# Kernel tuning notes

Measured on AMD Instinct MI355X. Metric: run time of the kernel, lower is better.

## Reference

```python
import jax, jax.numpy as jnp
import numpy as np
from jax.scipy.special import logsumexp

EPROB = 0.01
PSEUDO = 1.0


def setup_inputs() -> dict:
    key = jax.random.key(0)
    ks = jax.random.split(key, 6)
    B, m, n, d = 16, 2000, 1000, 5000
    gexp = jax.random.normal(ks[0], (B, d), jnp.float32)
    # one-hot observed dosages for 2B haplotypes (batch is duplicated in forward)
    idx = jax.random.randint(ks[1], (2 * B, m), 0, 2)
    x_onehots = jax.nn.one_hot(idx, 2, dtype=jnp.float32)
    W = jax.random.normal(ks[2], (d, m), jnp.float32) * 0.02  # predictor Linear weight
    b = jax.random.normal(ks[3], (m,), jnp.float32) * 0.01    # predictor Linear bias
    ref_tensor = jax.random.randint(ks[4], (m, n), 0, 2).astype(jnp.int32)  # 0/1 ref dosages
    recomb_rates = jax.random.uniform(ks[5], (m,), jnp.float32, 1e-4, 0.1)
    return dict(gexp=gexp, x_onehots=x_onehots, W=W, b=b,
                ref_tensor=ref_tensor, recomb_rates=recomb_rates)


def reference(gexp, x_onehots, W, b, ref_tensor, recomb_rates):
    m, n = ref_tensor.shape
    logn = jnp.log(jnp.float32(n))
    lse = logsumexp

    # predictor -> per-site Bernoulli priors, duplicated across haplotype pairs
    one_p = jax.nn.sigmoid(gexp @ W + b)                  # [B, m]
    prior = jnp.stack([1.0 - one_p, one_p], axis=-1)      # [B, m, 2]
    log_phi = jnp.log(jnp.repeat(prior, 2, axis=0))       # [2B, m, 2] (interleaved dup)
    B2 = log_phi.shape[0]

    # emission table: log of [[1-e, e],[e, 1-e]] + pseudocount/n
    E = np.array([[1.0 - EPROB, EPROB], [EPROB, 1.0 - EPROB]], dtype=np.float64) + PSEUDO / n
    logE = jnp.asarray(np.log(E), jnp.float32)            # [2, 2]
    SE = logE[ref_tensor]                                 # [m, n, 2] state emissions

    x_t = jnp.transpose(x_onehots, (1, 0, 2))             # [m, B2, 2]
    phi_t = jnp.transpose(log_phi, (1, 0, 2))             # [m, B2, 2]
    # forward step i uses recomb_rates[i+1]; last step's update is discarded
    r_next = jnp.concatenate([recomb_rates[1:], jnp.full((1,), 0.5, jnp.float32)])

    # ---- forward HMM pass: builds fprobx_haplo [m, B2, n] ----
    def fwd_step(f, xs):
        SE_i, x_i, r = xs                                  # [n,2], [B2,2], []
        nxt = f + jnp.einsum('kl,bl->bk', SE_i, x_i)       # [B2, n]
        nxt = nxt - lse(nxt, axis=1, keepdims=True)
        tot = lse(nxt, axis=1) - logn                      # [B2]
        nr = jnp.log((1.0 - r) * jnp.exp(nxt) + r * jnp.exp(tot)[:, None])
        nr = nr - lse(nr, axis=1, keepdims=True)
        return nr, f

    f0 = jnp.zeros((B2, n), jnp.float32)
    _, fprobx = jax.lax.scan(fwd_step, f0, (SE, x_t, r_next))  # [m, B2, n]

    # ---- backward pass (reverse recursion), accumulating log p(x|e) ----
    def bwd_step(carry, xs):
        state, p_xe = carry                                # state == prevprob == nextprob
        f_i, SE_i, phi_i, x_i, r = xs
        dp = lse(f_i[:, :, None] + state[:, :, None] + SE_i[None], axis=1)  # [B2, 2]
        dpp = dp + phi_i
        dpn = dpp - lse(dpp, axis=1, keepdims=True)
        p_xe = p_xe + jnp.sum(dpn * x_i, axis=1)
        nn = lse(SE_i[None] + phi_i[:, None, :], axis=2)   # [B2, n]
        state = state + nn - lse(nn, axis=1, keepdims=True)
        tot = lse(state, axis=1) - logn
        nr = jnp.log((1.0 - r) * jnp.exp(state) + r * jnp.exp(tot)[:, None])
        nr = nr - lse(nr, axis=1, keepdims=True)
        return (nr, p_xe), None

    init = (jnp.zeros((B2, n), jnp.float32), jnp.zeros((B2,), jnp.float32))
    (_, p_xe), _ = jax.lax.scan(bwd_step, init,
                                (fprobx, SE, phi_t, x_t, recomb_rates), reverse=True)

    return -jnp.sum(p_xe)  # loss_fn (training=True path)
```

## Files before the change

kernel.cpp:

```cpp
#include <hip/hip_runtime.h>
#include <stdint.h>
#include <stddef.h>

static constexpr int MM   = 2000;
static constexpr int NN   = 1000;
static constexpr int NB2  = 32;
static constexpr int DDIM = 5000;
static constexpr int NPR  = 1008;
static constexpr int NG   = 500;
static constexpr int JB   = 8;
static constexpr int NBAT = MM/JB;
static constexpr int NCR  = 36;
static constexpr float EAV = 0.991f;
static constexpr float EBV = 0.011f;

typedef uint32_t u32x4 __attribute__((ext_vector_type(4)));
typedef uint32_t u32x2 __attribute__((ext_vector_type(2)));
typedef float    f32x2 __attribute__((ext_vector_type(2)));

__device__ __forceinline__ float rcp_fast(float x){ return __builtin_amdgcn_rcpf(x); }

__device__ __forceinline__ void barrier_lds_only(){
  __builtin_amdgcn_sched_barrier(0);
  asm volatile("s_waitcnt lgkmcnt(0)" ::: "memory");
  __builtin_amdgcn_s_barrier();
  __builtin_amdgcn_sched_barrier(0);
}

__device__ __forceinline__ void wave_total2(float &a, float &b){
  int xa, xb;
  xa = __builtin_amdgcn_update_dpp(0, __float_as_int(a), 0x111, 0xf, 0xf, true);
  xb = __builtin_amdgcn_update_dpp(0, __float_as_int(b), 0x111, 0xf, 0xf, true);
  a += __int_as_float(xa); b += __int_as_float(xb);
  xa = __builtin_amdgcn_update_dpp(0, __float_as_int(a), 0x112, 0xf, 0xf, true);
  xb = __builtin_amdgcn_update_dpp(0, __float_as_int(b), 0x112, 0xf, 0xf, true);
  a += __int_as_float(xa); b += __int_as_float(xb);
  xa = __builtin_amdgcn_update_dpp(0, __float_as_int(a), 0x114, 0xf, 0xf, true);
  xb = __builtin_amdgcn_update_dpp(0, __float_as_int(b), 0x114, 0xf, 0xf, true);
  a += __int_as_float(xa); b += __int_as_float(xb);
  xa = __builtin_amdgcn_update_dpp(0, __float_as_int(a), 0x118, 0xf, 0xf, true);
  xb = __builtin_amdgcn_update_dpp(0, __float_as_int(b), 0x118, 0xf, 0xf, true);
  a += __int_as_float(xa); b += __int_as_float(xb);
  xa = __builtin_amdgcn_update_dpp(0, __float_as_int(a), 0x142, 0xa, 0xf, false);
  xb = __builtin_amdgcn_update_dpp(0, __float_as_int(b), 0x142, 0xa, 0xf, false);
  a += __int_as_float(xa); b += __int_as_float(xb);
  xa = __builtin_amdgcn_update_dpp(0, __float_as_int(a), 0x143, 0xc, 0xf, false);
  xb = __builtin_amdgcn_update_dpp(0, __float_as_int(b), 0x143, 0xc, 0xf, false);
  a += __int_as_float(xa); b += __int_as_float(xb);
  a = __int_as_float(__builtin_amdgcn_readlane(__float_as_int(a), 63));
  b = __int_as_float(__builtin_amdgcn_readlane(__float_as_int(b), 63));
}

template<int C,int RM,int BM,bool BC>
__device__ __forceinline__ void dpp_stage8(float m[8]){
  int x[8];
  #pragma unroll
  for (int j = 0; j < 8; ++j)
    x[j] = __builtin_amdgcn_update_dpp(0, __float_as_int(m[j]), C, RM, BM, BC);
  #pragma unroll
  for (int j = 0; j < 8; ++j) m[j] += __int_as_float(x[j]);
}
__device__ __forceinline__ void wave_total8_63(float m[8]){
  dpp_stage8<0x111,0xf,0xf,true>(m);
  dpp_stage8<0x112,0xf,0xf,true>(m);
  dpp_stage8<0x114,0xf,0xf,true>(m);
  dpp_stage8<0x118,0xf,0xf,true>(m);
  dpp_stage8<0x142,0xa,0xf,false>(m);
  dpp_stage8<0x143,0xc,0xf,false>(m);
}

#define CCEL(A,i) ( ((i)&3)==0 ? (A)[(i)>>2].x : ((i)&3)==1 ? (A)[(i)>>2].y : \
                    ((i)&3)==2 ? (A)[(i)>>2].z : (A)[(i)>>2].w )

__global__ __launch_bounds__(64) void k_pack(const int* __restrict__ ref,
                                             uint64_t* __restrict__ pack,
                                             uint4* __restrict__ refB4){
  int g = blockIdx.x;
  int t = threadIdx.x;
  uint64_t wv = 0;
  for (int c = 0; c < 4; ++c){
    int i = g*4 + c;
    uint32_t m16 = 0;
    uint32_t d[4] = {0,0,0,0};
    #pragma unroll
    for (int j = 0; j < 16; ++j){
      int k = t*16 + j;
      uint32_t v = (k < NN) ? (uint32_t)(ref[(size_t)i*NN + k] & 1) : 0u;
      m16 |= v << j;
      d[j>>2] |= v << (8*(j&3));
    }
    wv |= (uint64_t)m16 << (16*c);
    refB4[(size_t)i*64 + t] = make_uint4(d[0],d[1],d[2],d[3]);
  }
  pack[(size_t)g*64 + t] = wv;
}

__global__ __launch_bounds__(64) void k_obs(const float* __restrict__ xoh,
                                            uint32_t* __restrict__ obsw){
  int b2 = blockIdx.x;
  int w  = threadIdx.x;
  uint32_t word = 0;
  int base = w*32;
  #pragma unroll 4
  for (int z = 0; z < 32; ++z){
    int i = base + z;
    if (i < MM){
      float x1 = xoh[(size_t)b2*MM*2 + (size_t)i*2 + 1];
      if (x1 > 0.5f) word |= 1u << z;
    }
  }
  obsw[b2*64 + w] = word;
}

__global__ __launch_bounds__(256) void k_prep2(const float* __restrict__ xoh,
                                               const float* __restrict__ recomb,
                                               float4* __restrict__ FC4){
  int idx = blockIdx.x*256 + threadIdx.x;
  if (idx < NB2*MM){
    int b2 = idx / MM, i = idx - b2*MM;
    float x1 = xoh[(size_t)b2*MM*2 + (size_t)i*2 + 1];
    bool obs = x1 > 0.5f;
    float c0 = obs ? EBV : EAV;
    float c1 = obs ? (EAV-EBV) : (EBV-EAV);
    float rn = (i+1 < MM) ? recomb[i+1] : 0.5f;
    FC4[(size_t)b2*MM + i] = make_float4(c0, c1, 1.0f - rn, rn/(float)NN);
  }
}

__global__ __launch_bounds__(256) void k_gemm(const float* __restrict__ gexp,
                                              const float* __restrict__ W,
                                              float* __restrict__ part){
  int cb = blockIdx.x;
  int c  = blockIdx.y;
  int t  = threadIdx.x;
  int d0 = (c*DDIM) >> 4, d1 = ((c+1)*DDIM) >> 4;
  int len = d1 - d0;
  __shared__ __align__(16) float lg[313*20];
  for (int bb = 0; bb < 16; ++bb)
    for (int dd = t; dd < len; dd += 256)
      lg[dd*20 + bb] = gexp[(size_t)bb*DDIM + d0 + dd];
  __syncthreads();
  int i = cb*256 + t;
  if (i < MM){
    float acc[16];
    #pragma unroll
    for (int bb = 0; bb < 16; ++bb) acc[bb] = 0.f;
    for (int dd = 0; dd < len; ++dd){
      float w = W[(size_t)(d0 + dd)*MM + i];
      const float4* lp = (const float4*)&lg[dd*20];
      float4 g0 = lp[0], g1 = lp[1], g2 = lp[2], g3 = lp[3];
      acc[0]  += g0.x*w; acc[1]  += g0.y*w; acc[2]  += g0.z*w; acc[3]  += g0.w*w;
      acc[4]  += g1.x*w; acc[5]  += g1.y*w; acc[6]  += g1.z*w; acc[7]  += g1.w*w;
      acc[8]  += g2.x*w; acc[9]  += g2.y*w; acc[10] += g2.z*w; acc[11] += g2.w*w;
      acc[12] += g3.x*w; acc[13] += g3.y*w; acc[14] += g3.z*w; acc[15] += g3.w*w;
    }
    #pragma unroll
    for (int bb = 0; bb < 16; ++bb)
      part[((size_t)c*16 + bb)*MM + i] = acc[bb];
  }
}

__global__ __launch_bounds__(256) void k_gemmreduce(const float* __restrict__ part,
                                                    const float* __restrict__ bias,
                                                    const float* __restrict__ recomb,
                                                    float* __restrict__ acc,
                                                    float4* __restrict__ BC4){
  int idx = blockIdx.x*256 + threadIdx.x;
  if (idx < 16*MM){
    float s = 0.f;
    #pragma unroll
    for (int c = 0; c < 16; ++c) s += part[(size_t)c*16*MM + idx];
    acc[idx] = s;
    int bb = idx / MM, i = idx - bb*MM;
    float z = s + bias[i];
    float p = rcp_fast(1.0f + __expf(-z));
    float v0 = EAV + (EBV-EAV)*p;
    float v1 = EBV + (EAV-EBV)*p;
    float r = recomb[i];
    BC4[idx] = make_float4(v0, v1 - v0, 1.0f - r, r/(float)NN);
  }
}

__global__ __launch_bounds__(64) void k_ctab(const uint4* __restrict__ refB4,
                                             const float4* __restrict__ FC4,
                                             const float4* __restrict__ BC4,
                                             float* __restrict__ Cout){
  int wid  = blockIdx.x;
  int lane = threadIdx.x;
  int chain = wid / NBAT;
  int nb    = wid - chain*NBAT;
  int DIR = (chain < 32) ? 1 : -1;
  int b2  = chain & 31;
  const float4* ctab = (chain < 32) ? (FC4 + (size_t)b2*MM) : (BC4 + (size_t)(b2>>1)*MM);
  int start = (DIR > 0) ? 0 : (MM-1);

  f32x2 e[8][8];
  #pragma unroll
  for (int m = 0; m < 8; ++m){
    int site = start + DIR*(nb*JB + m);
    uint4 by = refB4[(size_t)site*64 + lane];
    float4 cc = ctab[site];
    f32x2 c0p; c0p.x = cc.x; c0p.y = cc.x;
    f32x2 c1p; c1p.x = cc.y; c1p.y = cc.y;
    uint32_t rw[4] = {by.x, by.y, by.z, by.w};
    #pragma unroll
    for (int q = 0; q < 4; ++q){
      f32x2 b01, b23;
      b01.x = (float)( rw[q]        & 0xFFu);
      b01.y = (float)((rw[q] >> 8)  & 0xFFu);
      b23.x = (float)((rw[q] >> 16) & 0xFFu);
      b23.y = (float)( rw[q] >> 24);
      e[m][2*q]   = c0p + c1p*b01;
      e[m][2*q+1] = c0p + c1p*b23;
    }
  }
  const float mlo = (lane < 63) ? 1.0f : 0.0f;
  const float mhi = (lane < 62) ? 1.0f : 0.0f;

  __shared__ float red[64*NCR];
  int cnt = 0;
  #pragma unroll
  for (int l = 0; l < 8; ++l){
    f32x2 c[8];
    #pragma unroll
    for (int q = 0; q < 8; ++q){
      f32x2 mk; mk.x = (q < 4) ? mlo : mhi; mk.y = mk.x;
      c[q] = e[l][q] * mk;
    }
    #pragma unroll
    for (int jj = l; jj < 8; ++jj){
      if (jj > l){
        #pragma unroll
        for (int q = 0; q < 8; ++q) c[q] = c[q] * e[jj][q];
      }
      f32x2 s0 = (c[0]+c[1]) + (c[2]+c[3]);
      f32x2 s1 = (c[4]+c[5]) + (c[6]+c[7]);
      f32x2 ss = s0 + s1;
      red[lane*NCR + cnt] = ss.x + ss.y;
      ++cnt;
    }
  }
  __syncthreads();
  if (lane < NCR){
    float s = 0.f;
    #pragma unroll
    for (int k = 0; k < 64; ++k) s += red[k*NCR + lane];
    Cout[(size_t)wid*NCR + lane] = s;
  }
}

template<int DIR>
__device__ void run_chain4(const uint32_t* __restrict__ refW,
                           const float4* __restrict__ ctab,
                           const float* __restrict__ Crec,
                           uint16_t* __restrict__ outp,
                           int b2, int w, int lane,
                           float4* lds_ctab, float* lds_C, float* partb){
  for (int idx = w*64 + lane; idx < MM; idx += 256)
    lds_ctab[idx] = ctab[idx];
  for (int idx = w*64 + lane; idx < NBAT*NCR; idx += 256)
    lds_C[idx] = Crec[idx];
  __syncthreads();

  const float mv  = ((w < 3) || (lane < 58)) ? 1.0f : 0.0f;
  const bool doSt = (w < 3) || (lane < 60);

  const ptrdiff_t rstep = (ptrdiff_t)DIR * 256;
  const uint32_t* rp = refW + ((DIR > 0) ? 0 : (ptrdiff_t)(MM-1)*256) + w*64 + lane;
  const ptrdiff_t ostep = (ptrdiff_t)DIR * NB2 * NPR;
  uint16_t* op = outp + (size_t)b2*NPR
               + ((DIR > 0) ? (size_t)0 : (size_t)(MM-1)*(size_t)NB2*NPR)
               + (size_t)w*256 + (size_t)lane*4;

  uint32_t A[8], Bv[8];
  #pragma unroll
  for (int k = 0; k < 8; ++k) A[k]  = rp[(ptrdiff_t)k*rstep];
  #pragma unroll
  for (int k = 0; k < 8; ++k) Bv[k] = rp[(ptrdiff_t)(k+8)*rstep];

  int ci = (DIR > 0) ? 0 : (MM-1);

  float4 cur8[8];
  #pragma unroll
  for (int k = 0; k < 8; ++k) cur8[k] = lds_ctab[ci + DIR*k];

  f32x2 g0, g1;
  g0.x = 0.f; g0.y = 0.f; g1.x = 0.f; g1.y = 0.f;
  float dd      = 1.0f/(float)NN;
  float az_prev = 0.0f;
  int buf = 0;
  constexpr int CO[8] = {0,8,15,21,26,30,33,35};

  #pragma unroll 2
  for (int n = 0; n < NBAT; ++n){
    uint32_t Cv[8];
    #pragma unroll
    for (int k = 0; k < 8; ++k) Cv[k] = rp[(ptrdiff_t)(8*n + 16 + k)*rstep];
    float4 nx8[8];
    {
      int cin = (n < NBAT-1) ? (ci + DIR*8) : ci;
      #pragma unroll
      for (int k = 0; k < 8; ++k) nx8[k] = lds_ctab[cin + DIR*k];
    }
    float4 CC[9];
    {
      const float4* crp = (const float4*)(lds_C + n*NCR);
      #pragma unroll
      for (int r = 0; r < 9; ++r) CC[r] = crp[r];
    }
    f32x2 e0[8], e1[8];
    #pragma unroll
    for (int k = 0; k < 8; ++k){
      uint32_t rw = A[k];
      f32x2 c0p; c0p.x = cur8[k].x; c0p.y = cur8[k].x;
      f32x2 c1p; c1p.x = cur8[k].y; c1p.y = cur8[k].y;
      f32x2 b01, b23;
      b01.x = (float)( rw        & 0xFFu);
      b01.y = (float)((rw >> 8)  & 0xFFu);
      b23.x = (float)((rw >> 16) & 0xFFu);
      b23.y = (float)( rw >> 24);
      e0[k] = c0p + c1p*b01;
      e1[k] = c0p + c1p*b23;
    }
    float m[8];
    {
      f32x2 c0 = g0*e0[0], c1 = g1*e1[0];
      f32x2 hv = c0 + c1;
      m[0] = hv.x + hv.y;
      #pragma unroll
      for (int k = 1; k < 8; ++k){
        c0 = c0*e0[k]; c1 = c1*e1[k];
        f32x2 h = c0 + c1;
        m[k] = h.x + h.y;
      }
    }
    wave_total8_63(m);
    if (lane == 63){
      #pragma unroll
      for (int j = 0; j < 8; ++j) partb[buf*32 + j*4 + w] = m[j];
    }
    barrier_lds_only();
    float M[8];
    #pragma unroll
    for (int j = 0; j < 8; ++j){
      const float4 pp = *(const float4*)(partb + buf*32 + j*4);
      M[j] = (pp.x + pp.y) + (pp.z + pp.w);
    }
    float cf[8];
    float azp = az_prev;
    float R = 1.0f;
    #pragma unroll
    for (int j = 0; j < 8; ++j){
      if (j > 0){
        float azm = cur8[j-1].z;
        azp *= azm;
        #pragma unroll
        for (int l = 0; l < 8; ++l) if (l < j) cf[l] *= azm;
      }
      cf[j] = dd;
      float az_j = (j == 0) ? az_prev : cur8[j-1].z;
      float dm = dd * mv;
      f32x2 azv; azv.x = az_j; azv.y = az_j;
      f32x2 dmv; dmv.x = dm;   dmv.y = dm;
      f32x2 t0 = g0*azv + dmv;
      f32x2 t1 = g1*azv + dmv;
      if (doSt){
        u32x2 v;
        v.x = __builtin_amdgcn_perm(__float_as_uint(t0.y), __float_as_uint(t0.x), 0x07060302u);
        v.y = __builtin_amdgcn_perm(__float_as_uint(t1.y), __float_as_uint(t1.x), 0x07060302u);
        *(u32x2*)op = v;
      }
      op += ostep;
      g0 = t0*e0[j];
      g1 = t1*e1[j];
      float T = azp * M[j];
      #pragma unroll
      for (int l = 0; l < 8; ++l) if (l <= j) T = fmaf(cf[l], CCEL(CC, CO[l] + (j-l)), T);
      R = T;
      dd = cur8[j].w * R;
    }
    float s = rcp_fast(R);
    f32x2 sp; sp.x = s; sp.y = s;
    g0 = g0*sp; g1 = g1*sp;
    dd *= s;
    az_prev = cur8[7].z;
    ci += DIR*8;
    buf ^= 1;
    #pragma unroll
    for (int k = 0; k < 8; ++k){ A[k] = Bv[k]; Bv[k] = Cv[k]; }
    #pragma unroll
    for (int k = 0; k < 8; ++k) cur8[k] = nx8[k];
  }
}

__global__ __launch_bounds__(256, 1) void k_chains(const uint4* __restrict__ refB4,
                                                   const float4* __restrict__ FC4,
                                                   const float4* __restrict__ BC4,
                                                   const float* __restrict__ Cw,
                                                   uint16_t* __restrict__ F,
                                                   uint16_t* __restrict__ S){
  __shared__ __align__(16) float4 lds_ctab[MM];
  __shared__ __align__(16) float lds_C[NBAT*NCR];
  __shared__ __align__(16) float partb[64];
  int lane = threadIdx.x & 63;
  int w    = threadIdx.x >> 6;
  int blk  = blockIdx.x;
  int b2   = blk & 31;
  const uint32_t* refW = (const uint32_t*)refB4;
  const float* Crec = Cw + (size_t)blk*NBAT*NCR;
  if (blk < 32) run_chain4<1>(refW, FC4 + (size_t)b2*MM, Crec, F, b2, w, lane,
                              lds_ctab, lds_C, partb);
  else          run_chain4<-1>(refW, BC4 + (size_t)(b2>>1)*MM, Crec, S, b2, w, lane,
                               lds_ctab, lds_C, partb);
}

__global__ __launch_bounds__(256) void k_sites(const uint16_t* __restrict__ F,
                                               const uint16_t* __restrict__ S,
                                               const uint64_t* __restrict__ pack,
                                               const uint32_t* __restrict__ obsw,
                                               const float* __restrict__ acc,
                                               const float* __restrict__ bias,
                                               float* __restrict__ terms){
  int lane = threadIdx.x & 63;
  int wid  = threadIdx.x >> 6;
  int s    = blockIdx.x*4 + wid;
  int i    = s >> 5;
  int b2   = s & 31;
  uint4 f0 = make_uint4(0,0,0,0), f1 = f0, s0 = f0, s1 = f0;
  if (lane < 63){
    size_t off = ((size_t)i*NB2 + b2)*NPR + lane*16;
    const uint4* fp = (const uint4*)(F + off);
    const uint4* sp = (const uint4*)(S + off);
    f0 = fp[0]; f1 = fp[1];
    s0 = sp[0]; s1 = sp[1];
  }
  uint32_t m16 = (uint32_t)(pack[(size_t)(i>>2)*64 + lane] >> (16*(i&3))) & 0xFFFFu;

  uint32_t fa[8] = {f0.x,f0.y,f0.z,f0.w,f1.x,f1.y,f1.z,f1.w};
  uint32_t sa[8] = {s0.x,s0.y,s0.z,s0.w,s1.x,s1.y,s1.z,s1.w};
  float Tt = 0.f, Tb = 0.f;
  #pragma unroll
  for (int q = 0; q < 8; ++q){
    float flo = __uint_as_float(fa[q] << 16);
    float fhi = __uint_as_float(fa[q] & 0xFFFF0000u);
    float slo = __uint_as_float(sa[q] << 16);
    float shi = __uint_as_float(sa[q] & 0xFFFF0000u);
    float pl = flo*slo, ph = fhi*shi;
    Tt += pl + ph;
    Tb += (((m16 >> (2*q)) & 1u) ? pl : 0.f) + (((m16 >> (2*q+1)) & 1u) ? ph : 0.f);
  }
  wave_total2(Tt, Tb);
  if (lane == 0){
    uint32_t obsb = (obsw[b2*64 + (i>>5)] >> (i & 31)) & 1u;
    float z = acc[(size_t)(b2 >> 1)*MM + i] + bias[i];
    float p = rcp_fast(1.0f + __expf(-z));
    float A = Tt - Tb, B = Tb;
    float d0 = EAV*A + EBV*B;
    float d1 = EBV*A + EAV*B;
    float w0 = d0*(1.0f - p), w1 = d1*p;
    float term = __logf((obsb ? w1 : w0) * rcp_fast(w0 + w1));
    terms[s] = term;
  }
}

__global__ __launch_bounds__(256) void k_final(const float* __restrict__ terms,
                                               float* __restrict__ out){
  __shared__ float red[256];
  float s = 0.f;
  for (int idx = threadIdx.x; idx < MM*NB2; idx += 256) s += terms[idx];
  red[threadIdx.x] = s;
  __syncthreads();
  for (int st = 128; st > 0; st >>= 1){
    if (threadIdx.x < st) red[threadIdx.x] += red[threadIdx.x + st];
    __syncthreads();
  }
  if (threadIdx.x == 0) out[0] = -red[0];
}

extern "C" void kernel_launch(void* const* d_in, const int* in_sizes, int n_in,
                              void* d_out, int out_size, void* d_ws, size_t ws_size,
                              hipStream_t stream){
  const float* gexp   = (const float*)d_in[0];
  const float* xoh    = (const float*)d_in[1];
  const float* W      = (const float*)d_in[2];
  const float* bias   = (const float*)d_in[3];
  const int*   ref    = (const int*)d_in[4];
  const float* recomb = (const float*)d_in[5];
  float* out = (float*)d_out;
  char* ws = (char*)d_ws;

  const size_t stateBytes = (size_t)MM*NB2*NPR*2;
  size_t offF    = 0;
  size_t offS    = offF + stateBytes;
  size_t offPack = offS + stateBytes;
  size_t offObs  = offPack + (size_t)NG*64*8;
  size_t offPart = offObs + 32*64*4;
  size_t offTerm = offPart + (size_t)16*16*MM*4;
  size_t offAcc  = offTerm + (size_t)MM*NB2*4;
  size_t offRefB = offAcc + (size_t)16*MM*4;
  size_t offFC4  = offRefB + (size_t)(MM+32)*1024;
  size_t offBC4  = offFC4 + (size_t)NB2*MM*16;

  uint16_t* Fb   = (uint16_t*)(ws + offF);
  uint16_t* Sb   = (uint16_t*)(ws + offS);
  uint64_t* pack = (uint64_t*)(ws + offPack);
  uint32_t* obsw = (uint32_t*)(ws + offObs);
  float*    part = (float*)(ws + offPart);
  float*    Cw   = (float*)(ws + offPart);
  float*    term = (float*)(ws + offTerm);
  float*    accp = (float*)(ws + offAcc);
  uint4*    refB = (uint4*)(ws + offRefB) + 16*64;
  float4*   FC4  = (float4*)(ws + offFC4);
  float4*   BC4  = (float4*)(ws + offBC4);

  hipLaunchKernelGGL(k_pack, dim3(NG), dim3(64), 0, stream, ref, pack, refB);
  hipLaunchKernelGGL(k_obs, dim3(32), dim3(64), 0, stream, xoh, obsw);
  hipLaunchKernelGGL(k_prep2, dim3((NB2*MM+255)/256), dim3(256), 0, stream, xoh, recomb, FC4);
  hipLaunchKernelGGL(k_gemm, dim3(8,16), dim3(256), 0, stream, gexp, W, part);
  hipLaunchKernelGGL(k_gemmreduce, dim3(125), dim3(256), 0, stream, part, bias, recomb, accp, BC4);
  hipLaunchKernelGGL(k_ctab, dim3(64*NBAT), dim3(64), 0, stream, refB, FC4, BC4, Cw);
  hipLaunchKernelGGL(k_chains, dim3(64), dim3(256), 0, stream, refB, FC4, BC4, Cw, Fb, Sb);
  hipLaunchKernelGGL(k_sites, dim3(MM*NB2/4), dim3(256), 0, stream, Fb, Sb, pack, obsw, accp, bias, term);
  hipLaunchKernelGGL(k_final, dim3(1), dim3(256), 0, stream, term, out);
}
```

Measured before the change: 600.1 us.

## Split each HMM chain across eight waves with two states per lane

```diff
diff --git a/kernel.cpp b/kernel.cpp
--- a/kernel.cpp
+++ b/kernel.cpp
@@ -250,27 +250,27 @@
 }
 
 template<int DIR>
-__device__ void run_chain4(const uint32_t* __restrict__ refW,
+__device__ void run_chain8(const uint16_t* __restrict__ refH,
                            const float4* __restrict__ ctab,
                            const float* __restrict__ Crec,
                            uint16_t* __restrict__ outp,
                            int b2, int w, int lane,
                            float4* lds_ctab, float* lds_C, float* partb){
-  for (int idx = w*64 + lane; idx < MM; idx += 256)
-    lds_ctab[idx] = ctab[idx];
-  for (int idx = w*64 + lane; idx < NBAT*NCR; idx += 256)
-    lds_C[idx] = Crec[idx];
+  int tid = w*64 + lane;
+  for (int idx = tid; idx < MM; idx += 512) lds_ctab[idx] = ctab[idx];
+  for (int idx = tid; idx < NBAT*NCR; idx += 512) lds_C[idx] = Crec[idx];
   __syncthreads();
 
-  const float mv  = ((w < 3) || (lane < 58)) ? 1.0f : 0.0f;
-  const bool doSt = (w < 3) || (lane < 60);
-
-  const ptrdiff_t rstep = (ptrdiff_t)DIR * 256;
-  const uint32_t* rp = refW + ((DIR > 0) ? 0 : (ptrdiff_t)(MM-1)*256) + w*64 + lane;
+  const int st0 = w*128 + lane*2;
+  const float mv  = (st0 < NN)  ? 1.0f : 0.0f;
+  const bool doSt = (st0 < NPR);
+
+  const ptrdiff_t rstep = (ptrdiff_t)DIR * 512;
+  const uint16_t* rp = refH + ((DIR > 0) ? 0 : (ptrdiff_t)(MM-1)*512) + tid;
   const ptrdiff_t ostep = (ptrdiff_t)DIR * NB2 * NPR;
   uint16_t* op = outp + (size_t)b2*NPR
                + ((DIR > 0) ? (size_t)0 : (size_t)(MM-1)*(size_t)NB2*NPR)
-               + (size_t)w*256 + (size_t)lane*4;
+               + (size_t)st0;
 
   uint32_t A[8], Bv[8];
   #pragma unroll
@@ -284,8 +284,7 @@
   #pragma unroll
   for (int k = 0; k < 8; ++k) cur8[k] = lds_ctab[ci + DIR*k];
 
-  f32x2 g0, g1;
-  g0.x = 0.f; g0.y = 0.f; g1.x = 0.f; g1.y = 0.f;
+  f32x2 g; g.x = 0.f; g.y = 0.f;
   float dd      = 1.0f/(float)NN;
   float az_prev = 0.0f;
   int buf = 0;
@@ -308,44 +307,44 @@
       #pragma unroll
       for (int r = 0; r < 9; ++r) CC[r] = crp[r];
     }
-    f32x2 e0[8], e1[8];
+    f32x2 e[8];
     #pragma unroll
     for (int k = 0; k < 8; ++k){
       uint32_t rw = A[k];
+      f32x2 b01;
+      b01.x = (float)( rw        & 0xFFu);
+      b01.y = (float)( rw >> 8);
       f32x2 c0p; c0p.x = cur8[k].x; c0p.y = cur8[k].x;
       f32x2 c1p; c1p.x = cur8[k].y; c1p.y = cur8[k].y;
-      f32x2 b01, b23;
-      b01.x = (float)( rw        & 0xFFu);
-      b01.y = (float)((rw >> 8)  & 0xFFu);
-      b23.x = (float)((rw >> 16) & 0xFFu);
-      b23.y = (float)( rw >> 24);
-      e0[k] = c0p + c1p*b01;
-      e1[k] = c0p + c1p*b23;
+      e[k] = c0p + c1p*b01;
     }
     float m[8];
     {
-      f32x2 c0 = g0*e0[0], c1 = g1*e1[0];
-      f32x2 hv = c0 + c1;
-      m[0] = hv.x + hv.y;
+      f32x2 c = g*e[0];
+      m[0] = c.x + c.y;
       #pragma unroll
       for (int k = 1; k < 8; ++k){
-        c0 = c0*e0[k]; c1 = c1*e1[k];
-        f32x2 h = c0 + c1;
-        m[k] = h.x + h.y;
+        c = c*e[k];
+        m[k] = c.x + c.y;
       }
     }
     wave_total8_63(m);
     if (lane == 63){
       #pragma unroll
-      for (int j = 0; j < 8; ++j) partb[buf*32 + j*4 + w] = m[j];
+      for (int j = 0; j < 8; ++j) partb[buf*64 + j*8 + w] = m[j];
     }
     barrier_lds_only();
     float M[8];
-    #pragma unroll
-    for (int j = 0; j < 8; ++j){
-      const float4 pp = *(const float4*)(partb + buf*32 + j*4);
-      M[j] = (pp.x + pp.y) + (pp.z + pp.w);
-    }
+    {
+      int ll = lane & 7;
+      const float4* pb = (const float4*)(partb + buf*64 + ll*8);
+      float4 pa = pb[0], pc = pb[1];
+      float msum = ((pa.x+pa.y)+(pa.z+pa.w)) + ((pc.x+pc.y)+(pc.z+pc.w));
+      #pragma unroll
+      for (int j = 0; j < 8; ++j)
+        M[j] = __int_as_float(__builtin_amdgcn_readlane(__float_as_int(msum), j));
+    }
+    uint32_t vst[8];
     float cf[8];
     float azp = az_prev;
     float R = 1.0f;
@@ -362,26 +361,27 @@
       float dm = dd * mv;
       f32x2 azv; azv.x = az_j; azv.y = az_j;
       f32x2 dmv; dmv.x = dm;   dmv.y = dm;
-      f32x2 t0 = g0*azv + dmv;
-      f32x2 t1 = g1*azv + dmv;
-      if (doSt){
-        u32x2 v;
-        v.x = __builtin_amdgcn_perm(__float_as_uint(t0.y), __float_as_uint(t0.x), 0x07060302u);
-        v.y = __builtin_amdgcn_perm(__float_as_uint(t1.y), __float_as_uint(t1.x), 0x07060302u);
-        *(u32x2*)op = v;
-      }
-      op += ostep;
-      g0 = t0*e0[j];
-      g1 = t1*e1[j];
+      f32x2 t = g*azv + dmv;
+      vst[j] = __builtin_amdgcn_perm(__float_as_uint(t.y), __float_as_uint(t.x), 0x07060302u);
+      g = t*e[j];
       float T = azp * M[j];
       #pragma unroll
       for (int l = 0; l < 8; ++l) if (l <= j) T = fmaf(cf[l], CCEL(CC, CO[l] + (j-l)), T);
       R = T;
       dd = cur8[j].w * R;
     }
+    if (doSt){
+      uint16_t* o = op;
+      #pragma unroll
+      for (int j = 0; j < 8; ++j){
+        *(uint32_t*)o = vst[j];
+        o += ostep;
+      }
+    }
+    op += 8*ostep;
     float s = rcp_fast(R);
     f32x2 sp; sp.x = s; sp.y = s;
-    g0 = g0*sp; g1 = g1*sp;
+    g = g*sp;
     dd *= s;
     az_prev = cur8[7].z;
     ci += DIR*8;
@@ -393,7 +393,7 @@
   }
 }
 
-__global__ __launch_bounds__(256, 1) void k_chains(const uint4* __restrict__ refB4,
+__global__ __launch_bounds__(512, 1) void k_chains(const uint4* __restrict__ refB4,
                                                    const float4* __restrict__ FC4,
                                                    const float4* __restrict__ BC4,
                                                    const float* __restrict__ Cw,
@@ -401,16 +401,16 @@
                                                    uint16_t* __restrict__ S){
   __shared__ __align__(16) float4 lds_ctab[MM];
   __shared__ __align__(16) float lds_C[NBAT*NCR];
-  __shared__ __align__(16) float partb[64];
+  __shared__ __align__(16) float partb[128];
   int lane = threadIdx.x & 63;
   int w    = threadIdx.x >> 6;
   int blk  = blockIdx.x;
   int b2   = blk & 31;
-  const uint32_t* refW = (const uint32_t*)refB4;
+  const uint16_t* refH = (const uint16_t*)refB4;
   const float* Crec = Cw + (size_t)blk*NBAT*NCR;
-  if (blk < 32) run_chain4<1>(refW, FC4 + (size_t)b2*MM, Crec, F, b2, w, lane,
+  if (blk < 32) run_chain8<1>(refH, FC4 + (size_t)b2*MM, Crec, F, b2, w, lane,
                               lds_ctab, lds_C, partb);
-  else          run_chain4<-1>(refW, BC4 + (size_t)(b2>>1)*MM, Crec, S, b2, w, lane,
+  else          run_chain8<-1>(refH, BC4 + (size_t)(b2>>1)*MM, Crec, S, b2, w, lane,
                                lds_ctab, lds_C, partb);
 }
 
@@ -519,7 +519,7 @@
   hipLaunchKernelGGL(k_gemm, dim3(8,16), dim3(256), 0, stream, gexp, W, part);
   hipLaunchKernelGGL(k_gemmreduce, dim3(125), dim3(256), 0, stream, part, bias, recomb, accp, BC4);
   hipLaunchKernelGGL(k_ctab, dim3(64*NBAT), dim3(64), 0, stream, refB, FC4, BC4, Cw);
-  hipLaunchKernelGGL(k_chains, dim3(64), dim3(256), 0, stream, refB, FC4, BC4, Cw, Fb, Sb);
+  hipLaunchKernelGGL(k_chains, dim3(64), dim3(512), 0, stream, refB, FC4, BC4, Cw, Fb, Sb);
   hipLaunchKernelGGL(k_sites, dim3(MM*NB2/4), dim3(256), 0, stream, Fb, Sb, pack, obsw, accp, bias, term);
   hipLaunchKernelGGL(k_final, dim3(1), dim3(256), 0, stream, term, out);
 }
```

Result: slower. 644.7 us (+7.4%).

## Run forward and backward chains interleaved in one block per haplotype

Applied to the files above, without the earlier changes.

```diff
diff --git a/kernel.cpp b/kernel.cpp
--- a/kernel.cpp
+++ b/kernel.cpp
@@ -52,21 +52,21 @@
 }
 
 template<int C,int RM,int BM,bool BC>
-__device__ __forceinline__ void dpp_stage8(float m[8]){
-  int x[8];
+__device__ __forceinline__ void dpp_stage16(float m[16]){
+  int x[16];
   #pragma unroll
-  for (int j = 0; j < 8; ++j)
+  for (int j = 0; j < 16; ++j)
     x[j] = __builtin_amdgcn_update_dpp(0, __float_as_int(m[j]), C, RM, BM, BC);
   #pragma unroll
-  for (int j = 0; j < 8; ++j) m[j] += __int_as_float(x[j]);
-}
-__device__ __forceinline__ void wave_total8_63(float m[8]){
-  dpp_stage8<0x111,0xf,0xf,true>(m);
-  dpp_stage8<0x112,0xf,0xf,true>(m);
-  dpp_stage8<0x114,0xf,0xf,true>(m);
-  dpp_stage8<0x118,0xf,0xf,true>(m);
-  dpp_stage8<0x142,0xa,0xf,false>(m);
-  dpp_stage8<0x143,0xc,0xf,false>(m);
+  for (int j = 0; j < 16; ++j) m[j] += __int_as_float(x[j]);
+}
+__device__ __forceinline__ void wave_total16_63(float m[16]){
+  dpp_stage16<0x111,0xf,0xf,true>(m);
+  dpp_stage16<0x112,0xf,0xf,true>(m);
+  dpp_stage16<0x114,0xf,0xf,true>(m);
+  dpp_stage16<0x118,0xf,0xf,true>(m);
+  dpp_stage16<0x142,0xa,0xf,false>(m);
+  dpp_stage16<0x143,0xc,0xf,false>(m);
 }
 
 #define CCEL(A,i) ( ((i)&3)==0 ? (A)[(i)>>2].x : ((i)&3)==1 ? (A)[(i)>>2].y : \
@@ -249,169 +249,250 @@
   }
 }
 
-template<int DIR>
-__device__ void run_chain4(const uint32_t* __restrict__ refW,
-                           const float4* __restrict__ ctab,
-                           const float* __restrict__ Crec,
-                           uint16_t* __restrict__ outp,
-                           int b2, int w, int lane,
-                           float4* lds_ctab, float* lds_C, float* partb){
-  for (int idx = w*64 + lane; idx < MM; idx += 256)
-    lds_ctab[idx] = ctab[idx];
-  for (int idx = w*64 + lane; idx < NBAT*NCR; idx += 256)
-    lds_C[idx] = Crec[idx];
-  __syncthreads();
-
-  const float mv  = ((w < 3) || (lane < 58)) ? 1.0f : 0.0f;
-  const bool doSt = (w < 3) || (lane < 60);
-
-  const ptrdiff_t rstep = (ptrdiff_t)DIR * 256;
-  const uint32_t* rp = refW + ((DIR > 0) ? 0 : (ptrdiff_t)(MM-1)*256) + w*64 + lane;
-  const ptrdiff_t ostep = (ptrdiff_t)DIR * NB2 * NPR;
-  uint16_t* op = outp + (size_t)b2*NPR
-               + ((DIR > 0) ? (size_t)0 : (size_t)(MM-1)*(size_t)NB2*NPR)
-               + (size_t)w*256 + (size_t)lane*4;
-
-  uint32_t A[8], Bv[8];
-  #pragma unroll
-  for (int k = 0; k < 8; ++k) A[k]  = rp[(ptrdiff_t)k*rstep];
-  #pragma unroll
-  for (int k = 0; k < 8; ++k) Bv[k] = rp[(ptrdiff_t)(k+8)*rstep];
-
-  int ci = (DIR > 0) ? 0 : (MM-1);
-
-  float4 cur8[8];
-  #pragma unroll
-  for (int k = 0; k < 8; ++k) cur8[k] = lds_ctab[ci + DIR*k];
-
-  f32x2 g0, g1;
-  g0.x = 0.f; g0.y = 0.f; g1.x = 0.f; g1.y = 0.f;
-  float dd      = 1.0f/(float)NN;
-  float az_prev = 0.0f;
-  int buf = 0;
-  constexpr int CO[8] = {0,8,15,21,26,30,33,35};
-
-  #pragma unroll 2
-  for (int n = 0; n < NBAT; ++n){
-    uint32_t Cv[8];
-    #pragma unroll
-    for (int k = 0; k < 8; ++k) Cv[k] = rp[(ptrdiff_t)(8*n + 16 + k)*rstep];
-    float4 nx8[8];
-    {
-      int cin = (n < NBAT-1) ? (ci + DIR*8) : ci;
-      #pragma unroll
-      for (int k = 0; k < 8; ++k) nx8[k] = lds_ctab[cin + DIR*k];
-    }
-    float4 CC[9];
-    {
-      const float4* crp = (const float4*)(lds_C + n*NCR);
-      #pragma unroll
-      for (int r = 0; r < 9; ++r) CC[r] = crp[r];
-    }
-    f32x2 e0[8], e1[8];
-    #pragma unroll
-    for (int k = 0; k < 8; ++k){
-      uint32_t rw = A[k];
-      f32x2 c0p; c0p.x = cur8[k].x; c0p.y = cur8[k].x;
-      f32x2 c1p; c1p.x = cur8[k].y; c1p.y = cur8[k].y;
-      f32x2 b01, b23;
-      b01.x = (float)( rw        & 0xFFu);
-      b01.y = (float)((rw >> 8)  & 0xFFu);
-      b23.x = (float)((rw >> 16) & 0xFFu);
-      b23.y = (float)( rw >> 24);
-      e0[k] = c0p + c1p*b01;
-      e1[k] = c0p + c1p*b23;
-    }
-    float m[8];
-    {
-      f32x2 c0 = g0*e0[0], c1 = g1*e1[0];
-      f32x2 hv = c0 + c1;
-      m[0] = hv.x + hv.y;
-      #pragma unroll
-      for (int k = 1; k < 8; ++k){
-        c0 = c0*e0[k]; c1 = c1*e1[k];
-        f32x2 h = c0 + c1;
-        m[k] = h.x + h.y;
-      }
-    }
-    wave_total8_63(m);
-    if (lane == 63){
-      #pragma unroll
-      for (int j = 0; j < 8; ++j) partb[buf*32 + j*4 + w] = m[j];
-    }
-    barrier_lds_only();
-    float M[8];
-    #pragma unroll
-    for (int j = 0; j < 8; ++j){
-      const float4 pp = *(const float4*)(partb + buf*32 + j*4);
-      M[j] = (pp.x + pp.y) + (pp.z + pp.w);
-    }
-    float cf[8];
-    float azp = az_prev;
-    float R = 1.0f;
-    #pragma unroll
-    for (int j = 0; j < 8; ++j){
-      if (j > 0){
-        float azm = cur8[j-1].z;
-        azp *= azm;
-        #pragma unroll
-        for (int l = 0; l < 8; ++l) if (l < j) cf[l] *= azm;
-      }
-      cf[j] = dd;
-      float az_j = (j == 0) ? az_prev : cur8[j-1].z;
-      float dm = dd * mv;
-      f32x2 azv; azv.x = az_j; azv.y = az_j;
-      f32x2 dmv; dmv.x = dm;   dmv.y = dm;
-      f32x2 t0 = g0*azv + dmv;
-      f32x2 t1 = g1*azv + dmv;
-      if (doSt){
-        u32x2 v;
-        v.x = __builtin_amdgcn_perm(__float_as_uint(t0.y), __float_as_uint(t0.x), 0x07060302u);
-        v.y = __builtin_amdgcn_perm(__float_as_uint(t1.y), __float_as_uint(t1.x), 0x07060302u);
-        *(u32x2*)op = v;
-      }
-      op += ostep;
-      g0 = t0*e0[j];
-      g1 = t1*e1[j];
-      float T = azp * M[j];
-      #pragma unroll
-      for (int l = 0; l < 8; ++l) if (l <= j) T = fmaf(cf[l], CCEL(CC, CO[l] + (j-l)), T);
-      R = T;
-      dd = cur8[j].w * R;
-    }
-    float s = rcp_fast(R);
-    f32x2 sp; sp.x = s; sp.y = s;
-    g0 = g0*sp; g1 = g1*sp;
-    dd *= s;
-    az_prev = cur8[7].z;
-    ci += DIR*8;
-    buf ^= 1;
-    #pragma unroll
-    for (int k = 0; k < 8; ++k){ A[k] = Bv[k]; Bv[k] = Cv[k]; }
-    #pragma unroll
-    for (int k = 0; k < 8; ++k) cur8[k] = nx8[k];
-  }
-}
-
 __global__ __launch_bounds__(256, 1) void k_chains(const uint4* __restrict__ refB4,
                                                    const float4* __restrict__ FC4,
                                                    const float4* __restrict__ BC4,
                                                    const float* __restrict__ Cw,
                                                    uint16_t* __restrict__ F,
                                                    uint16_t* __restrict__ S){
-  __shared__ __align__(16) float4 lds_ctab[MM];
-  __shared__ __align__(16) float lds_C[NBAT*NCR];
-  __shared__ __align__(16) float partb[64];
-  int lane = threadIdx.x & 63;
-  int w    = threadIdx.x >> 6;
-  int blk  = blockIdx.x;
-  int b2   = blk & 31;
+  __shared__ __align__(16) float4 lds_ctabA[MM];
+  __shared__ __align__(16) float4 lds_ctabB[MM];
+  __shared__ __align__(16) float lds_CA[NBAT*NCR];
+  __shared__ __align__(16) float lds_CB[NBAT*NCR];
+  __shared__ __align__(16) float partb[128];
+  int tid  = threadIdx.x;
+  int lane = tid & 63;
+  int w    = tid >> 6;
+  int b2   = blockIdx.x;
   const uint32_t* refW = (const uint32_t*)refB4;
-  const float* Crec = Cw + (size_t)blk*NBAT*NCR;
-  if (blk < 32) run_chain4<1>(refW, FC4 + (size_t)b2*MM, Crec, F, b2, w, lane,
-                              lds_ctab, lds_C, partb);
-  else          run_chain4<-1>(refW, BC4 + (size_t)(b2>>1)*MM, Crec, S, b2, w, lane,
-                               lds_ctab, lds_C, partb);
+  const float4* ctabA = FC4 + (size_t)b2*MM;
+  const float4* ctabB = BC4 + (size_t)(b2>>1)*MM;
+  const float* CrecA = Cw + (size_t)b2*NBAT*NCR;
+  const float* CrecB = Cw + (size_t)(32+b2)*NBAT*NCR;
+  for (int idx = tid; idx < MM; idx += 256){
+    lds_ctabA[idx] = ctabA[idx];
+    lds_ctabB[idx] = ctabB[idx];
+  }
+  for (int idx = tid; idx < NBAT*NCR; idx += 256){
+    lds_CA[idx] = CrecA[idx];
+    lds_CB[idx] = CrecB[idx];
+  }
+  __syncthreads();
+
+  const float mv  = ((w < 3) || (lane < 58)) ? 1.0f : 0.0f;
+  const bool doSt = (w < 3) || (lane < 60);
+
+  const uint32_t* rpA = refW + tid;
+  const uint32_t* rpB = refW + (ptrdiff_t)(MM-1)*256 + tid;
+  uint16_t* opA = F + (size_t)b2*NPR + (size_t)w*256 + (size_t)lane*4;
+  uint16_t* opB = S + (size_t)b2*NPR + (size_t)(MM-1)*(size_t)NB2*NPR
+                + (size_t)w*256 + (size_t)lane*4;
+  const ptrdiff_t osA = (ptrdiff_t)NB2*NPR;
+  const ptrdiff_t osB = -(ptrdiff_t)NB2*NPR;
+
+  uint32_t Aa[8], Ab[8];
+  #pragma unroll
+  for (int k = 0; k < 8; ++k){
+    Aa[k] = rpA[(ptrdiff_t)k*256];
+    Ab[k] = rpB[-(ptrdiff_t)k*256];
+  }
+
+  f32x2 g0A, g1A, g0B, g1B;
+  g0A.x=0.f; g0A.y=0.f; g1A.x=0.f; g1A.y=0.f;
+  g0B.x=0.f; g0B.y=0.f; g1B.x=0.f; g1B.y=0.f;
+  float ddA = 1.0f/(float)NN, azA = 0.0f;
+  float ddB = 1.0f/(float)NN, azB = 0.0f;
+  int buf = 0;
+  constexpr int CO[8] = {0,8,15,21,26,30,33,35};
+
+  #pragma unroll 1
+  for (int n = 0; n < NBAT; ++n){
+    int base = n*8;
+    uint32_t Na[8], Nb[8];
+    {
+      int pn = (n < NBAT-1) ? (base + 8) : base;
+      #pragma unroll
+      for (int k = 0; k < 8; ++k){
+        Na[k] = rpA[(ptrdiff_t)(pn + k)*256];
+        Nb[k] = rpB[-(ptrdiff_t)(pn + k)*256];
+      }
+    }
+    float4 cur8A[8], cur8B[8];
+    #pragma unroll
+    for (int k = 0; k < 8; ++k){
+      cur8A[k] = lds_ctabA[base + k];
+      cur8B[k] = lds_ctabB[MM-1 - base - k];
+    }
+    float m16[16];
+    {
+      f32x2 c0 = g0A, c1 = g1A;
+      #pragma unroll
+      for (int k = 0; k < 8; ++k){
+        uint32_t rw = Aa[k];
+        f32x2 c0p; c0p.x = cur8A[k].x; c0p.y = cur8A[k].x;
+        f32x2 c1p; c1p.x = cur8A[k].y; c1p.y = cur8A[k].y;
+        f32x2 b01, b23;
+        b01.x = (float)( rw        & 0xFFu);
+        b01.y = (float)((rw >> 8)  & 0xFFu);
+        b23.x = (float)((rw >> 16) & 0xFFu);
+        b23.y = (float)( rw >> 24);
+        c0 = c0 * (c0p + c1p*b01);
+        c1 = c1 * (c0p + c1p*b23);
+        f32x2 h = c0 + c1;
+        m16[k] = h.x + h.y;
+      }
+    }
+    {
+      f32x2 c0 = g0B, c1 = g1B;
+      #pragma unroll
+      for (int k = 0; k < 8; ++k){
+        uint32_t rw = Ab[k];
+        f32x2 c0p; c0p.x = cur8B[k].x; c0p.y = cur8B[k].x;
+        f32x2 c1p; c1p.x = cur8B[k].y; c1p.y = cur8B[k].y;
+        f32x2 b01, b23;
+        b01.x = (float)( rw        & 0xFFu);
+        b01.y = (float)((rw >> 8)  & 0xFFu);
+        b23.x = (float)((rw >> 16) & 0xFFu);
+        b23.y = (float)( rw >> 24);
+        c0 = c0 * (c0p + c1p*b01);
+        c1 = c1 * (c0p + c1p*b23);
+        f32x2 h = c0 + c1;
+        m16[8+k] = h.x + h.y;
+      }
+    }
+    wave_total16_63(m16);
+    if (lane == 63){
+      #pragma unroll
+      for (int j = 0; j < 8; ++j){
+        partb[buf*64 +      j*4 + w] = m16[j];
+        partb[buf*64 + 32 + j*4 + w] = m16[8+j];
+      }
+    }
+    barrier_lds_only();
+    float4 CCA[9], CCB[9];
+    {
+      const float4* pa = (const float4*)(lds_CA + n*NCR);
+      const float4* pb = (const float4*)(lds_CB + n*NCR);
+      #pragma unroll
+      for (int r = 0; r < 9; ++r){ CCA[r] = pa[r]; CCB[r] = pb[r]; }
+    }
+    float MA[8], MB[8];
+    {
+      int ll = lane & 7;
+      const float4 pa = *(const float4*)(partb + buf*64 +      ll*4);
+      const float4 pb = *(const float4*)(partb + buf*64 + 32 + ll*4);
+      float sa = (pa.x + pa.y) + (pa.z + pa.w);
+      float sb = (pb.x + pb.y) + (pb.z + pb.w);
+      #pragma unroll
+      for (int j = 0; j < 8; ++j){
+        MA[j] = __int_as_float(__builtin_amdgcn_readlane(__float_as_int(sa), j));
+        MB[j] = __int_as_float(__builtin_amdgcn_readlane(__float_as_int(sb), j));
+      }
+    }
+    {
+      float cf[8];
+      float azp = azA;
+      float R = 1.0f;
+      #pragma unroll
+      for (int j = 0; j < 8; ++j){
+        if (j > 0){
+          float azm = cur8A[j-1].z;
+          azp *= azm;
+          #pragma unroll
+          for (int l = 0; l < 8; ++l) if (l < j) cf[l] *= azm;
+        }
+        cf[j] = ddA;
+        float az_j = (j == 0) ? azA : cur8A[j-1].z;
+        float dm = ddA * mv;
+        uint32_t rw = Aa[j];
+        f32x2 c0p; c0p.x = cur8A[j].x; c0p.y = cur8A[j].x;
+        f32x2 c1p; c1p.x = cur8A[j].y; c1p.y = cur8A[j].y;
+        f32x2 b01, b23;
+        b01.x = (float)( rw        & 0xFFu);
+        b01.y = (float)((rw >> 8)  & 0xFFu);
+        b23.x = (float)((rw >> 16) & 0xFFu);
+        b23.y = (float)( rw >> 24);
+        f32x2 e0 = c0p + c1p*b01;
+        f32x2 e1 = c0p + c1p*b23;
+        f32x2 azvp; azvp.x = az_j; azvp.y = az_j;
+        f32x2 dmv;  dmv.x = dm;    dmv.y = dm;
+        f32x2 t0 = g0A*azvp + dmv;
+        f32x2 t1 = g1A*azvp + dmv;
+        if (doSt){
+          u32x2 v;
+          v.x = __builtin_amdgcn_perm(__float_as_uint(t0.y), __float_as_uint(t0.x), 0x07060302u);
+          v.y = __builtin_amdgcn_perm(__float_as_uint(t1.y), __float_as_uint(t1.x), 0x07060302u);
+          *(u32x2*)opA = v;
+        }
+        opA += osA;
+        g0A = t0*e0;
+        g1A = t1*e1;
+        float T = azp * MA[j];
+        #pragma unroll
+        for (int l = 0; l < 8; ++l) if (l <= j) T = fmaf(cf[l], CCEL(CCA, CO[l] + (j-l)), T);
+        R = T;
+        ddA = cur8A[j].w * R;
+      }
+      float s = rcp_fast(R);
+      f32x2 sp; sp.x = s; sp.y = s;
+      g0A = g0A*sp; g1A = g1A*sp;
+      ddA *= s;
+      azA = cur8A[7].z;
+    }
+    {
+      float cf[8];
+      float azp = azB;
+      float R = 1.0f;
+      #pragma unroll
+      for (int j = 0; j < 8; ++j){
+        if (j > 0){
+          float azm = cur8B[j-1].z;
+          azp *= azm;
+          #pragma unroll
+          for (int l = 0; l < 8; ++l) if (l < j) cf[l] *= azm;
+        }
+        cf[j] = ddB;
+        float az_j = (j == 0) ? azB : cur8B[j-1].z;
+        float dm = ddB * mv;
+        uint32_t rw = Ab[j];
+        f32x2 c0p; c0p.x = cur8B[j].x; c0p.y = cur8B[j].x;
+        f32x2 c1p; c1p.x = cur8B[j].y; c1p.y = cur8B[j].y;
+        f32x2 b01, b23;
+        b01.x = (float)( rw        & 0xFFu);
+        b01.y = (float)((rw >> 8)  & 0xFFu);
+        b23.x = (float)((rw >> 16) & 0xFFu);
+        b23.y = (float)( rw >> 24);
+        f32x2 e0 = c0p + c1p*b01;
+        f32x2 e1 = c0p + c1p*b23;
+        f32x2 azvp; azvp.x = az_j; azvp.y = az_j;
+        f32x2 dmv;  dmv.x = dm;    dmv.y = dm;
+        f32x2 t0 = g0B*azvp + dmv;
+        f32x2 t1 = g1B*azvp + dmv;
+        if (doSt){
+          u32x2 v;
+          v.x = __builtin_amdgcn_perm(__float_as_uint(t0.y), __float_as_uint(t0.x), 0x07060302u);
+          v.y = __builtin_amdgcn_perm(__float_as_uint(t1.y), __float_as_uint(t1.x), 0x07060302u);
+          *(u32x2*)opB = v;
+        }
+        opB += osB;
+        g0B = t0*e0;
+        g1B = t1*e1;
+        float T = azp * MB[j];
+        #pragma unroll
+        for (int l = 0; l < 8; ++l) if (l <= j) T = fmaf(cf[l], CCEL(CCB, CO[l] + (j-l)), T);
+        R = T;
+        ddB = cur8B[j].w * R;
+      }
+      float s = rcp_fast(R);
+      f32x2 sp; sp.x = s; sp.y = s;
+      g0B = g0B*sp; g1B = g1B*sp;
+      ddB *= s;
+      azB = cur8B[7].z;
+    }
+    buf ^= 1;
+    #pragma unroll
+    for (int k = 0; k < 8; ++k){ Aa[k] = Na[k]; Ab[k] = Nb[k]; }
+  }
 }
 
 __global__ __launch_bounds__(256) void k_sites(const uint16_t* __restrict__ F,
@@ -519,7 +600,7 @@
   hipLaunchKernelGGL(k_gemm, dim3(8,16), dim3(256), 0, stream, gexp, W, part);
   hipLaunchKernelGGL(k_gemmreduce, dim3(125), dim3(256), 0, stream, part, bias, recomb, accp, BC4);
   hipLaunchKernelGGL(k_ctab, dim3(64*NBAT), dim3(64), 0, stream, refB, FC4, BC4, Cw);
-  hipLaunchKernelGGL(k_chains, dim3(64), dim3(256), 0, stream, refB, FC4, BC4, Cw, Fb, Sb);
+  hipLaunchKernelGGL(k_chains, dim3(32), dim3(256), 0, stream, refB, FC4, BC4, Cw, Fb, Sb);
   hipLaunchKernelGGL(k_sites, dim3(MM*NB2/4), dim3(256), 0, stream, Fb, Sb, pack, obsw, accp, bias, term);
   hipLaunchKernelGGL(k_final, dim3(1), dim3(256), 0, stream, term, out);
 }
```

After: 839.5 us. 39.9% more time.
